# Optimization experiments

Measured on AMD Instinct MI355X. Metric: run time of the kernel, lower is better.

## Reference

```python
import jax, jax.numpy as jnp
import numpy as np

B, S, C = 32, 512, 384
MAX_LEN = 4096
MAX_DUR = 16


def setup_inputs() -> dict:
    key = jax.random.key(0)
    kx, kd = jax.random.split(key)
    x = jax.random.normal(kx, (B, S, C), dtype=jnp.float32)
    durations = jax.random.randint(kd, (B, S), 0, MAX_DUR, dtype=jnp.int32)
    return {"x": x, "durations": durations, "max_length": MAX_LEN}


def reference(x, durations, max_length):
    # Round (no-op for int durations, kept for faithfulness to torch.round().long())
    d = jnp.round(durations.astype(jnp.float32)).astype(jnp.int32)  # [B, S]
    # _limit_durations is equivalent to clipping the cumulative sum at max_length:
    # the first token crossing max_length gets truncated, all later tokens zeroed.
    ends = jnp.clip(jnp.cumsum(d, axis=1), 0, max_length)          # [B, S]
    total = ends[:, -1]                                            # [B]
    t = jnp.arange(max_length, dtype=jnp.int32)                    # [T]
    # frame t belongs to phoneme j where starts[j] <= t < ends[j];
    # searchsorted(ends, t, 'right') skips zero-duration tokens automatically.
    idx = jax.vmap(lambda e: jnp.searchsorted(e, t, side='right'))(ends)  # [B, T]
    mel_masks = t[None, :] >= total[:, None]                       # [B, T] True = pad
    idx_c = jnp.clip(idx, 0, x.shape[1] - 1)
    expanded = jnp.take_along_axis(x, idx_c[:, :, None], axis=1)   # [B, T, C]
    expanded = jnp.where(mel_masks[:, :, None], jnp.zeros((), x.dtype), expanded)
    return expanded, mel_masks
```

## Files before the change

### kernel.cpp

```cpp
#include <hip/hip_runtime.h>

#define BATCH 32
#define SEQ 512
#define CH4 96
#define MAXL 4096
#define FPB 8
#define CPB 64
#define THREADS 128

typedef float v4f __attribute__((ext_vector_type(4)));
typedef int   v4i __attribute__((ext_vector_type(4)));

__global__ __launch_bounds__(THREADS) void lr_fused(
    const v4f* __restrict__ x,
    const v4i* __restrict__ dur4,
    const int* __restrict__ max_len_p,
    v4f* __restrict__ out,
    float* __restrict__ out_mask)
{
    __shared__ int s_end[SEQ];

    const int tid   = threadIdx.x;
    const int bid   = blockIdx.x;
    const int b     = bid >> 6;
    const int chunk = bid & (CPB - 1);
    const int j0    = chunk * FPB;

    v4f vx[FPB];
    if (tid < CH4) {
        const v4f* xp = x + ((size_t)(b * SEQ + j0)) * CH4 + tid;
        #pragma unroll
        for (int fr = 0; fr < FPB; ++fr) vx[fr] = xp[fr * CH4];
    }

    if (tid < 64) {
        const v4i* dp = dur4 + b * (SEQ / 4) + tid * 2;
        v4i d0 = dp[0], d1 = dp[1];
        int lane_sum = d0.x + d0.y + d0.z + d0.w + d1.x + d1.y + d1.z + d1.w;
        int incl = lane_sum;
        #pragma unroll
        for (int off = 1; off < 64; off <<= 1) {
            int v = __shfl_up(incl, off, 64);
            if (tid >= off) incl += v;
        }
        int cum = incl - lane_sum;
        const int maxlen = max_len_p[0];
        const int base = tid * 8;
        cum += d0.x; s_end[base + 0] = min(cum, maxlen);
        cum += d0.y; s_end[base + 1] = min(cum, maxlen);
        cum += d0.z; s_end[base + 2] = min(cum, maxlen);
        cum += d0.w; s_end[base + 3] = min(cum, maxlen);
        cum += d1.x; s_end[base + 4] = min(cum, maxlen);
        cum += d1.y; s_end[base + 5] = min(cum, maxlen);
        cum += d1.z; s_end[base + 6] = min(cum, maxlen);
        cum += d1.w; s_end[base + 7] = min(cum, maxlen);
    }
    __syncthreads();

    const int st0   = j0 ? s_end[j0 - 1] : 0;
    const int e7    = s_end[j0 + FPB - 1];
    const int total = s_end[SEQ - 1];

    if (tid < e7 - st0) out_mask[(b << 12) + st0 + tid] = 0.0f;

    if (tid < CH4) {
        v4f* const ob_base = out + ((size_t)(b << 12)) * CH4 + tid;
        #pragma unroll
        for (int fr = 0; fr < FPB; ++fr) {
            const int jj = j0 + fr;
            const int e  = s_end[jj];
            const int st = jj ? s_end[jj - 1] : 0;
            v4f v = vx[fr];
            v4f* ob = ob_base + (size_t)st * CH4;
            for (int t = st; t < e; ++t) {
                *ob = v;
                ob += CH4;
            }
        }
    }

    const v4f zero = (v4f){0.f, 0.f, 0.f, 0.f};
    for (int t = total + chunk; t < MAXL; t += CPB) {
        if (tid < CH4)
            out[((size_t)(b << 12) + t) * CH4 + tid] = zero;
        else if (tid == CH4)
            out_mask[(b << 12) + t] = 1.0f;
    }
}

extern "C" void kernel_launch(void* const* d_in, const int* in_sizes, int n_in,
                              void* d_out, int out_size, void* d_ws, size_t ws_size,
                              hipStream_t stream) {
    const v4f* x = (const v4f*)d_in[0];
    const v4i* dur4 = (const v4i*)d_in[1];
    const int* max_len_p = (const int*)d_in[2];
    float* out = (float*)d_out;
    float* out_mask = out + (size_t)BATCH * MAXL * CH4 * 4;

    lr_fused<<<BATCH * CPB, THREADS, 0, stream>>>(
        x, dur4, max_len_p, (v4f*)out, out_mask);
}
```

Before: 215.8 us.

## Switch from per-phoneme scatter to per-output-slab gather with binary search

```diff
diff --git a/kernel.cpp b/kernel.cpp
--- a/kernel.cpp
+++ b/kernel.cpp
@@ -4,14 +4,15 @@
 #define SEQ 512
 #define CH4 96
 #define MAXL 4096
-#define FPB 8
-#define CPB 64
-#define THREADS 128
+#define THREADS 256
+#define SLABS 64
+#define ROWS_PB 64
+#define ITERS 24
 
 typedef float v4f __attribute__((ext_vector_type(4)));
 typedef int   v4i __attribute__((ext_vector_type(4)));
 
-__global__ __launch_bounds__(THREADS) void lr_fused(
+__global__ __launch_bounds__(THREADS) void lr_gather(
     const v4f* __restrict__ x,
     const v4i* __restrict__ dur4,
     const int* __restrict__ max_len_p,
@@ -19,19 +20,13 @@
     float* __restrict__ out_mask)
 {
     __shared__ int s_end[SEQ];
+    __shared__ int s_src[ROWS_PB];
 
-    const int tid   = threadIdx.x;
-    const int bid   = blockIdx.x;
-    const int b     = bid >> 6;
-    const int chunk = bid & (CPB - 1);
-    const int j0    = chunk * FPB;
-
-    v4f vx[FPB];
-    if (tid < CH4) {
-        const v4f* xp = x + ((size_t)(b * SEQ + j0)) * CH4 + tid;
-        #pragma unroll
-        for (int fr = 0; fr < FPB; ++fr) vx[fr] = xp[fr * CH4];
-    }
+    const int tid  = threadIdx.x;
+    const int bid  = blockIdx.x;
+    const int b    = bid >> 6;
+    const int slab = bid & (SLABS - 1);
+    const int r0   = slab * ROWS_PB;
 
     if (tid < 64) {
         const v4i* dp = dur4 + b * (SEQ / 4) + tid * 2;
@@ -57,34 +52,37 @@
     }
     __syncthreads();
 
-    const int st0   = j0 ? s_end[j0 - 1] : 0;
-    const int e7    = s_end[j0 + FPB - 1];
     const int total = s_end[SEQ - 1];
 
-    if (tid < e7 - st0) out_mask[(b << 12) + st0 + tid] = 0.0f;
+    if (tid < ROWS_PB) {
+        const int t = r0 + tid;
+        int lo = 0, hi = SEQ;
+        #pragma unroll
+        for (int s = 0; s < 10; ++s) {
+            int mid = (lo + hi) >> 1;
+            mid = min(mid, SEQ - 1);
+            const bool le = (s_end[mid] <= t);
+            lo = le ? mid + 1 : lo;
+            hi = le ? hi : mid;
+        }
+        s_src[tid] = (t < total) ? lo : -1;
+        out_mask[(b << 12) + t] = (t >= total) ? 1.0f : 0.0f;
+    }
+    __syncthreads();
 
-    if (tid < CH4) {
-        v4f* const ob_base = out + ((size_t)(b << 12)) * CH4 + tid;
-        #pragma unroll
-        for (int fr = 0; fr < FPB; ++fr) {
-            const int jj = j0 + fr;
-            const int e  = s_end[jj];
-            const int st = jj ? s_end[jj - 1] : 0;
-            v4f v = vx[fr];
-            v4f* ob = ob_base + (size_t)st * CH4;
-            for (int t = st; t < e; ++t) {
-                *ob = v;
-                ob += CH4;
-            }
-        }
-    }
+    const v4f* xb = x + (size_t)b * (SEQ * CH4);
+    v4f* ob = out + ((size_t)(b << 12) + r0) * CH4;
+    const v4f vzero = (v4f){0.f, 0.f, 0.f, 0.f};
 
-    const v4f zero = (v4f){0.f, 0.f, 0.f, 0.f};
-    for (int t = total + chunk; t < MAXL; t += CPB) {
-        if (tid < CH4)
-            out[((size_t)(b << 12) + t) * CH4 + tid] = zero;
-        else if (tid == CH4)
-            out_mask[(b << 12) + t] = 1.0f;
+    #pragma unroll 6
+    for (int it = 0; it < ITERS; ++it) {
+        const int g = it * THREADS + tid;
+        const int r = g / CH4;
+        const int c = g - r * CH4;
+        const int j = s_src[r];
+        v4f v = vzero;
+        if (j >= 0) v = xb[j * CH4 + c];
+        ob[g] = v;
     }
 }
 
@@ -97,6 +95,6 @@
     float* out = (float*)d_out;
     float* out_mask = out + (size_t)BATCH * MAXL * CH4 * 4;
 
-    lr_fused<<<BATCH * CPB, THREADS, 0, stream>>>(
+    lr_gather<<<BATCH * SLABS, THREADS, 0, stream>>>(
         x, dur4, max_len_p, (v4f*)out, out_mask);
 }
```

Result: slower. 231.3 us (+7.1%).
